# Kernel tuning notes

Hardware: AMD Instinct MI355X
Metric: run time of the kernel (lower is better)

The kernel has to match this reference:

```python
import jax, jax.numpy as jnp
import numpy as np

DIM = 1024
HEADS = 8
DIM_HEAD = 64
INNER = HEADS * DIM_HEAD  # 512


def setup_inputs() -> dict:
    key = jax.random.key(0)
    k1, k2, k3, k4 = jax.random.split(key, 4)
    x = jax.random.normal(k1, (4, 4096, DIM), dtype=jnp.float32)
    # torch nn.Linear weights: [out_features, in_features]
    w_qkv = jax.random.normal(k2, (INNER * 3, DIM), dtype=jnp.float32) * (DIM ** -0.5)
    w_out = jax.random.normal(k3, (DIM, INNER), dtype=jnp.float32) * (INNER ** -0.5)
    b_out = jax.random.normal(k4, (DIM,), dtype=jnp.float32) * 0.01
    return {"x": x, "w_qkv": w_qkv, "w_out": w_out, "b_out": b_out}


def reference(x, w_qkv, w_out, b_out):
    b, n, _ = x.shape
    h, dh = HEADS, DIM_HEAD
    qkv = x @ w_qkv.T  # [b, n, 3*inner]
    q, k, v = jnp.split(qkv, 3, axis=-1)
    # [b, n, inner] -> [b, h, n, dh]
    reshape = lambda t: t.reshape(b, n, h, dh).transpose(0, 2, 1, 3)
    q, k, v = reshape(q), reshape(k), reshape(v)
    k = jax.nn.softmax(k, axis=-1)
    context = jnp.einsum('bhnd,bhne->bhde', k, v)   # [b, h, dh, dh]
    out = jnp.einsum('bhnd,bhde->bhne', q, context)  # [b, h, n, dh]
    out = out.transpose(0, 2, 1, 3).reshape(b, n, h * dh)
    return out @ w_out.T + b_out
```

## Files before the change

### kernel.cpp

```cpp
#include <hip/hip_runtime.h>
#include <hip/hip_bf16.h>

using bf16 = __hip_bfloat16;
typedef __attribute__((ext_vector_type(8))) short short8;
typedef __attribute__((ext_vector_type(4))) float floatx4;

#define NB 4
#define NSEQ 4096
#define DIM 1024
#define INNER 512
#define TOK (NB * NSEQ)


__device__ inline unsigned short f2bf(float x) {
  union { bf16 h; unsigned short u; } c; c.h = __float2bfloat16(x); return c.u;
}
__device__ inline float bf2f(unsigned short u) {
  return __uint_as_float((unsigned)u << 16);
}
__device__ inline uint4 pack8(const float4 a, const float4 b) {
  union { uint4 u; unsigned short h[8]; } p;
  p.h[0] = f2bf(a.x); p.h[1] = f2bf(a.y); p.h[2] = f2bf(a.z); p.h[3] = f2bf(a.w);
  p.h[4] = f2bf(b.x); p.h[5] = f2bf(b.y); p.h[6] = f2bf(b.z); p.h[7] = f2bf(b.w);
  return p.u;
}

__device__ inline void gload_lds16(const bf16* g, bf16* ldsbase) {
  __builtin_amdgcn_global_load_lds(
      (const __attribute__((address_space(1))) void*)g,
      (__attribute__((address_space(3))) void*)ldsbase, 16, 0, 0);
}

__global__ __launch_bounds__(256)
void fused_prep(const float* __restrict__ x, const float* __restrict__ w_qkv,
                bf16* __restrict__ xb, bf16* __restrict__ wkvb,
                bf16* __restrict__ wqT) {
  const int tid = threadIdx.x;
  const int blk = blockIdx.x;

  if (blk < 8192) {
    const size_t i = (size_t)blk * 256 + tid;
    const float* src = x + i * 8;
    *(uint4*)(xb + i * 8) = pack8(((const float4*)src)[0], ((const float4*)src)[1]);
  } else if (blk < 8704) {
    const size_t i = (size_t)(blk - 8192) * 256 + tid;
    const float* src = w_qkv + (size_t)INNER * DIM + i * 8;
    *(uint4*)(wkvb + i * 8) = pack8(((const float4*)src)[0], ((const float4*)src)[1]);
  } else {
    __shared__ unsigned short t[64 * 68];
    const int q  = blk - 8704;
    const int c0 = (q & 15) * 64;
    const int r0 = (q >> 4) * 64;
#pragma unroll
    for (int l = 0; l < 4; ++l) {
      const int s = l * 256 + tid;
      const int row = s >> 4, col4 = s & 15;
      const float4 v = *(const float4*)(w_qkv + (size_t)(r0 + row) * 1024 + c0 + col4 * 4);
      t[row * 68 + col4 * 4 + 0] = f2bf(v.x);
      t[row * 68 + col4 * 4 + 1] = f2bf(v.y);
      t[row * 68 + col4 * 4 + 2] = f2bf(v.z);
      t[row * 68 + col4 * 4 + 3] = f2bf(v.w);
    }
    __syncthreads();
#pragma unroll
    for (int l = 0; l < 2; ++l) {
      const int s = l * 256 + tid;
      const int cc = s >> 3, g = s & 7;
      union { uint4 u; unsigned short h[8]; } o;
#pragma unroll
      for (int u = 0; u < 8; ++u) o.h[u] = t[(g * 8 + u) * 68 + cc];
      *(uint4*)((unsigned short*)wqT + (size_t)(c0 + cc) * 512 + r0 + g * 8) = o.u;
    }
  }
}

__global__ __launch_bounds__(256, 4)
void kv_softmax_ctx(const bf16* __restrict__ A, const bf16* __restrict__ Wkv,
                    float* __restrict__ ctx_part) {
  __shared__ __align__(16) char smem[33280];
  bf16* As = (bf16*)smem;
  bf16* Bs = (bf16*)(smem + 16384);
  unsigned short* skT = (unsigned short*)smem;
  unsigned short* vT  = (unsigned short*)(smem + 16640);

  const int tid    = threadIdx.x;
  const int p      = blockIdx.x;
  const int h      = (p >> 3) & 7;
  const int m_tile = (p & 7) + (p >> 6) * 8;
  const int m0     = m_tile * 128;

  const int wave = tid >> 6;
  const int lane = tid & 63;
  const int wr   = (wave >> 1) * 64;
  const int wc   = (wave & 1) * 64;
  const int quad = lane >> 4;
  const int r16  = lane & 15;
  const int rxor = r16 & 7;
  const int lrow = lane >> 3;
  const int lcol = lane & 7;
  const int gchunk = lcol ^ lrow;

  floatx4 acc[4][4];
#pragma unroll
  for (int i = 0; i < 4; ++i)
#pragma unroll
    for (int j = 0; j < 4; ++j) acc[i][j] = (floatx4)0.0f;

  for (int kt = 0; kt < 16; ++kt) {
    const int k0 = kt << 6;
#pragma unroll
    for (int t = 0; t < 4; ++t) {
      const int s   = wave * 4 + t;
      const int row = s * 8 + lrow;
      const int badd = (s * 8 >= 64) ? (448 + h * 64) : (h * 64);
      gload_lds16(A   + (size_t)(m0 + row) * 1024 + k0 + gchunk * 8, As + s * 512);
      gload_lds16(Wkv + (size_t)(badd + row) * 1024 + k0 + gchunk * 8, Bs + s * 512);
    }
    __syncthreads();
#pragma unroll
    for (int kk = 0; kk < 64; kk += 32) {
      const int cbase = kk >> 3;
      short8 af[4], bfg[4];
#pragma unroll
      for (int i = 0; i < 4; ++i)
        af[i] = *(const short8*)(As + (wr + i * 16 + r16) * 64 + (((quad + cbase) ^ rxor) << 3));
#pragma unroll
      for (int j = 0; j < 4; ++j)
        bfg[j] = *(const short8*)(Bs + (wc + j * 16 + r16) * 64 + (((quad + cbase) ^ rxor) << 3));
#pragma unroll
      for (int i = 0; i < 4; ++i)
#pragma unroll
        for (int j = 0; j < 4; ++j)
          acc[i][j] = __builtin_amdgcn_mfma_f32_16x16x32_bf16(af[i], bfg[j], acc[i][j], 0, 0, 0);
    }
    __syncthreads();
  }

  const int rowbase = wr + quad * 4;
  if ((wave & 1) == 0) {
#pragma unroll
    for (int i = 0; i < 4; ++i)
#pragma unroll
      for (int reg = 0; reg < 4; ++reg) {
        float kf[4];
#pragma unroll
        for (int j = 0; j < 4; ++j) kf[j] = bf2f(f2bf(acc[i][j][reg]));
        float mx = fmaxf(fmaxf(kf[0], kf[1]), fmaxf(kf[2], kf[3]));
        mx = fmaxf(mx, __shfl_xor(mx, 1, 64));
        mx = fmaxf(mx, __shfl_xor(mx, 2, 64));
        mx = fmaxf(mx, __shfl_xor(mx, 4, 64));
        mx = fmaxf(mx, __shfl_xor(mx, 8, 64));
        float e[4]; float s = 0.0f;
#pragma unroll
        for (int j = 0; j < 4; ++j) { e[j] = __expf(kf[j] - mx); s += e[j]; }
        s += __shfl_xor(s, 1, 64);
        s += __shfl_xor(s, 2, 64);
        s += __shfl_xor(s, 4, 64);
        s += __shfl_xor(s, 8, 64);
        const float inv = 1.0f / s;
        const int row = rowbase + i * 16 + reg;
#pragma unroll
        for (int j = 0; j < 4; ++j)
          skT[(j * 16 + r16) * 130 + row] = f2bf(e[j] * inv);
      }
  } else {
#pragma unroll
    for (int i = 0; i < 4; ++i)
#pragma unroll
      for (int reg = 0; reg < 4; ++reg) {
        const int row = rowbase + i * 16 + reg;
#pragma unroll
        for (int j = 0; j < 4; ++j)
          vT[(j * 16 + r16) * 130 + row] = f2bf(acc[i][j][reg]);
      }
  }
  __syncthreads();

  const int d0 = wave * 16;
  floatx4 cacc[4];
#pragma unroll
  for (int j = 0; j < 4; ++j) cacc[j] = (floatx4)0.0f;
#pragma unroll
  for (int kk = 0; kk < 4; ++kk) {
    const int kof = kk * 32 + quad * 8;
    union { short8 v; unsigned u[4]; } afr;
    {
      const unsigned* qa = (const unsigned*)(skT + (d0 + r16) * 130 + kof);
      afr.u[0] = qa[0]; afr.u[1] = qa[1]; afr.u[2] = qa[2]; afr.u[3] = qa[3];
    }
#pragma unroll
    for (int j = 0; j < 4; ++j) {
      union { short8 v; unsigned u[4]; } bfr;
      const unsigned* qb = (const unsigned*)(vT + (j * 16 + r16) * 130 + kof);
      bfr.u[0] = qb[0]; bfr.u[1] = qb[1]; bfr.u[2] = qb[2]; bfr.u[3] = qb[3];
      cacc[j] = __builtin_amdgcn_mfma_f32_16x16x32_bf16(afr.v, bfr.v, cacc[j], 0, 0, 0);
    }
  }

  float* cg = ctx_part + (size_t)(m_tile * 8 + h) * 4096;
#pragma unroll
  for (int j = 0; j < 4; ++j) {
    const int e = j * 16 + r16;
#pragma unroll
    for (int r = 0; r < 4; ++r) {
      const int d = d0 + quad * 4 + r;
      cg[d * 64 + e] = cacc[j][r];
    }
  }
}

__global__ __launch_bounds__(256)
void build_m2(const float* __restrict__ w_out, const float* __restrict__ ctx_part,
              bf16* __restrict__ M2) {
  __shared__ unsigned short wo_s[128 * 68];
  __shared__ __align__(16) float ctx_s[4096];

  const int tid = threadIdx.x;
  const int bh  = blockIdx.y;
  const int b   = bh >> 3, h = bh & 7;
  const int o0  = blockIdx.x * 128;

#pragma unroll
  for (int l = 0; l < 8; ++l) {
    const int s = l * 256 + tid;
    const int row = s >> 4, col4 = s & 15;
    const float4 v = *(const float4*)(w_out + (size_t)(o0 + row) * 512 + h * 64 + col4 * 4);
    wo_s[row * 68 + col4 * 4 + 0] = f2bf(v.x);
    wo_s[row * 68 + col4 * 4 + 1] = f2bf(v.y);
    wo_s[row * 68 + col4 * 4 + 2] = f2bf(v.z);
    wo_s[row * 68 + col4 * 4 + 3] = f2bf(v.w);
  }
  const float4* cg = (const float4*)(ctx_part + (size_t)(b * 256 + h) * 4096);
#pragma unroll
  for (int l = 0; l < 4; ++l) {
    const int idx = l * 256 + tid;
    float4 s = make_float4(0.f, 0.f, 0.f, 0.f);
#pragma unroll
    for (int sl = 0; sl < 32; ++sl) {
      const float4 v = cg[(size_t)sl * 8192 + idx];
      s.x += v.x; s.y += v.y; s.z += v.z; s.w += v.w;
    }
    ((float4*)ctx_s)[idx] = s;
  }
  __syncthreads();

  const int o_loc = tid & 127;
  const int dbase = (tid >> 7) * 32;
  float acc[32];
#pragma unroll
  for (int d = 0; d < 32; ++d) acc[d] = 0.0f;

  for (int e = 0; e < 64; ++e) {
    const float wf = bf2f(wo_s[o_loc * 68 + e]);
#pragma unroll
    for (int d = 0; d < 32; ++d)
      acc[d] += wf * ctx_s[(dbase + d) * 64 + e];
  }

  union { uint4 u[4]; unsigned short hh[32]; } o;
#pragma unroll
  for (int d = 0; d < 32; ++d) o.hh[d] = f2bf(acc[d]);
  unsigned short* dst = (unsigned short*)M2 + (size_t)(b * 1024 + o0 + o_loc) * 512 + h * 64 + dbase;
#pragma unroll
  for (int i = 0; i < 4; ++i) ((uint4*)dst)[i] = o.u[i];
}

template <typename TO>
__global__ __launch_bounds__(256, 4)
void gemm_bt(const bf16* __restrict__ A, int lda,
             const bf16* __restrict__ W, int mTiles,
             TO* __restrict__ C, int ldc, int K,
             TO* __restrict__ Calt, int msplit) {
  __shared__ __align__(16) bf16 As[128 * 64];
  __shared__ __align__(16) bf16 Bs[128 * 64];

  const int tid    = threadIdx.x;
  const int p      = blockIdx.x;
  const int m_tile = p % mTiles;
  const int n_tile = p / mTiles;
  const int m0     = m_tile * 128;
  const int n0     = n_tile * 128;

  const int wave = tid >> 6;
  const int lane = tid & 63;
  const int wr   = (wave >> 1) * 64;
  const int wc   = (wave & 1) * 64;
  const int quad = lane >> 4;
  const int r16  = lane & 15;
  const int rxor = r16 & 7;
  const int lrow = lane >> 3;
  const int lcol = lane & 7;
  const int gchunk = lcol ^ lrow;

  floatx4 acc[4][4];
#pragma unroll
  for (int i = 0; i < 4; ++i)
#pragma unroll
    for (int j = 0; j < 4; ++j) acc[i][j] = (floatx4)0.0f;

  const int ksteps = K >> 6;
  for (int kt = 0; kt < ksteps; ++kt) {
    const int k0 = kt << 6;
#pragma unroll
    for (int t = 0; t < 4; ++t) {
      const int s   = wave * 4 + t;
      const int row = s * 8 + lrow;
      gload_lds16(A + (size_t)(m0 + row) * lda + k0 + gchunk * 8, As + s * 512);
      gload_lds16(W + (size_t)(n0 + row) * K   + k0 + gchunk * 8, Bs + s * 512);
    }
    __syncthreads();
#pragma unroll
    for (int kk = 0; kk < 64; kk += 32) {
      const int cbase = kk >> 3;
      short8 af[4], bfg[4];
#pragma unroll
      for (int i = 0; i < 4; ++i)
        af[i] = *(const short8*)(As + (wr + i * 16 + r16) * 64 + (((quad + cbase) ^ rxor) << 3));
#pragma unroll
      for (int j = 0; j < 4; ++j)
        bfg[j] = *(const short8*)(Bs + (wc + j * 16 + r16) * 64 + (((quad + cbase) ^ rxor) << 3));
#pragma unroll
      for (int i = 0; i < 4; ++i)
#pragma unroll
        for (int j = 0; j < 4; ++j)
          acc[i][j] = __builtin_amdgcn_mfma_f32_16x16x32_bf16(af[i], bfg[j], acc[i][j], 0, 0, 0);
    }
    __syncthreads();
  }

  TO* Cb = C; int radj = 0;
  if (Calt && m0 >= msplit) { Cb = Calt; radj = msplit; }
#pragma unroll
  for (int j = 0; j < 4; ++j) {
    const int col = n0 + wc + j * 16 + r16;
#pragma unroll
    for (int i = 0; i < 4; ++i) {
      const int rowb = m0 + wr + i * 16 + quad * 4 - radj;
#pragma unroll
      for (int r = 0; r < 4; ++r)
        Cb[(size_t)(rowb + r) * ldc + col] = __float2bfloat16(acc[i][j][r]);
    }
  }
}

__global__ __launch_bounds__(256, 4)
void gemm_f32a(const float* __restrict__ A,
               const bf16* __restrict__ W, size_t wbatch,
               const bf16* __restrict__ Walt,
               const float* __restrict__ bias,
               float* __restrict__ C, int ldc) {
  __shared__ __align__(16) bf16 As[128 * 64];
  __shared__ __align__(16) bf16 Bs[128 * 64];

  const int tid    = threadIdx.x;
  const int p      = blockIdx.x;
  const int n_tile = (p >> 3) & 7;
  const int m_tile = (p & 7) + (p >> 6) * 8;
  const int m0 = m_tile * 128, n0 = n_tile * 128;
  const int batch = m_tile >> 5;
  const bf16* Wp = (batch == 3 && Walt) ? Walt : W + (size_t)batch * wbatch;

  const int wave = tid >> 6;
  const int lane = tid & 63;
  const int wr   = (wave >> 1) * 64;
  const int wc   = (wave & 1) * 64;
  const int quad = lane >> 4;
  const int r16  = lane & 15;
  const int rxor = r16 & 7;
  const int lrow = lane >> 3;
  const int lcol = lane & 7;
  const int gchunk = lcol ^ lrow;
  const int wb = wave * 8 + lrow;

  const float* Ax = A + (size_t)(m0 + wb) * 1024 + lcol * 8;

  floatx4 acc[4][4];
#pragma unroll
  for (int i = 0; i < 4; ++i)
#pragma unroll
    for (int j = 0; j < 4; ++j) acc[i][j] = (floatx4)0.0f;

  for (int kt = 0; kt < 16; ++kt) {
    const int k0 = kt << 6;
#pragma unroll
    for (int t = 0; t < 4; ++t) {
      const int s   = wave * 4 + t;
      const int row = s * 8 + lrow;
      gload_lds16(Wp + (size_t)(n0 + row) * 1024 + k0 + gchunk * 8, Bs + s * 512);
    }
    float4 rA[8];
#pragma unroll
    for (int l = 0; l < 4; ++l) {
      rA[2 * l]     = *(const float4*)(Ax + (size_t)l * 32768 + k0);
      rA[2 * l + 1] = *(const float4*)(Ax + (size_t)l * 32768 + k0 + 4);
    }
#pragma unroll
    for (int l = 0; l < 4; ++l) {
      const int row = l * 32 + wb;
      *(uint4*)(As + row * 64 + ((lcol ^ lrow) << 3)) = pack8(rA[2 * l], rA[2 * l + 1]);
    }
    __syncthreads();
#pragma unroll
    for (int kk = 0; kk < 64; kk += 32) {
      const int cbase = kk >> 3;
      short8 af[4], bfg[4];
#pragma unroll
      for (int i = 0; i < 4; ++i)
        af[i] = *(const short8*)(As + (wr + i * 16 + r16) * 64 + (((quad + cbase) ^ rxor) << 3));
#pragma unroll
      for (int j = 0; j < 4; ++j)
        bfg[j] = *(const short8*)(Bs + (wc + j * 16 + r16) * 64 + (((quad + cbase) ^ rxor) << 3));
#pragma unroll
      for (int i = 0; i < 4; ++i)
#pragma unroll
        for (int j = 0; j < 4; ++j)
          acc[i][j] = __builtin_amdgcn_mfma_f32_16x16x32_bf16(af[i], bfg[j], acc[i][j], 0, 0, 0);
    }
    __syncthreads();
  }

#pragma unroll
  for (int j = 0; j < 4; ++j) {
    const int col = n0 + wc + j * 16 + r16;
    const float bv = bias[col];
#pragma unroll
    for (int i = 0; i < 4; ++i) {
      const int rowb = m0 + wr + i * 16 + quad * 4;
#pragma unroll
      for (int r = 0; r < 4; ++r)
        C[(size_t)(rowb + r) * ldc + col] = acc[i][j][r] + bv;
    }
  }
}

extern "C" void kernel_launch(void* const* d_in, const int* in_sizes, int n_in,
                              void* d_out, int out_size, void* d_ws, size_t ws_size,
                              hipStream_t stream) {
  const float* x     = (const float*)d_in[0];
  const float* w_qkv = (const float*)d_in[1];
  const float* w_out = (const float*)d_in[2];
  const float* b_out = (const float*)d_in[3];
  float* out = (float*)d_out;

  char* wbuf = (char*)d_in[1];
  char* obuf = (char*)d_out;

  bf16*  xb   = (bf16*)obuf;
  float* ctxp = (float*)(obuf + (size_t)33554432);
  bf16*  wkvb = (bf16*)(obuf + (size_t)50331648);
  bf16*  M2   = (bf16*)(obuf + (size_t)52428800);
  bf16*  wqT  = (bf16*)(obuf + (size_t)56623104);
  bf16*  W2   = (bf16*)wbuf;
  bf16*  W2b3 = (bf16*)d_in[2];

  fused_prep<<<8832, 256, 0, stream>>>(x, w_qkv, xb, wkvb, wqT);

  kv_softmax_ctx<<<1024, 256, 0, stream>>>(xb, wkvb, ctxp);

  build_m2<<<dim3(8, 32), 256, 0, stream>>>(w_out, ctxp, M2);

  gemm_bt<bf16><<<256, 256, 0, stream>>>(
      M2, 512, wqT, 32, W2, 1024, 512, W2b3, 3072);

  gemm_f32a<<<1024, 256, 0, stream>>>(
      x, W2, (size_t)1048576, W2b3, b_out, out, DIM);
}
```

Before: 264.3 us.

## Drop x bf16 pre-conversion; compute KV via f32-input GEMM then separate softmax-context kernel

The full x-to-bf16 conversion pass in prep is removed. K/V are now produced by the fp32-A GEMM kernel (converting x on load) and written to a bf16 buffer. A new softmax_context kernel then reads K/V, applies the softmax and accumulates the per-slice contexts, and build_m2 is adjusted to sum 16 partial slices. This avoids writing and re-reading a bf16 copy of x, but adds a write and read of a K/V intermediate and one more launch.

Result: faster. 256.6 us (-2.9%).

```diff
diff --git a/kernel.cpp b/kernel.cpp
--- a/kernel.cpp
+++ b/kernel.cpp
@@ -32,23 +32,18 @@
 }
 
 __global__ __launch_bounds__(256)
-void fused_prep(const float* __restrict__ x, const float* __restrict__ w_qkv,
-                bf16* __restrict__ xb, bf16* __restrict__ wkvb,
+void fused_prep(const float* __restrict__ w_qkv, bf16* __restrict__ wkvb,
                 bf16* __restrict__ wqT) {
   const int tid = threadIdx.x;
   const int blk = blockIdx.x;
 
-  if (blk < 8192) {
+  if (blk < 512) {
     const size_t i = (size_t)blk * 256 + tid;
-    const float* src = x + i * 8;
-    *(uint4*)(xb + i * 8) = pack8(((const float4*)src)[0], ((const float4*)src)[1]);
-  } else if (blk < 8704) {
-    const size_t i = (size_t)(blk - 8192) * 256 + tid;
     const float* src = w_qkv + (size_t)INNER * DIM + i * 8;
     *(uint4*)(wkvb + i * 8) = pack8(((const float4*)src)[0], ((const float4*)src)[1]);
   } else {
     __shared__ unsigned short t[64 * 68];
-    const int q  = blk - 8704;
+    const int q  = blk - 512;
     const int c0 = (q & 15) * 64;
     const int r0 = (q >> 4) * 64;
 #pragma unroll
@@ -74,281 +69,13 @@
   }
 }
 
-__global__ __launch_bounds__(256, 4)
-void kv_softmax_ctx(const bf16* __restrict__ A, const bf16* __restrict__ Wkv,
-                    float* __restrict__ ctx_part) {
-  __shared__ __align__(16) char smem[33280];
-  bf16* As = (bf16*)smem;
-  bf16* Bs = (bf16*)(smem + 16384);
-  unsigned short* skT = (unsigned short*)smem;
-  unsigned short* vT  = (unsigned short*)(smem + 16640);
-
-  const int tid    = threadIdx.x;
-  const int p      = blockIdx.x;
-  const int h      = (p >> 3) & 7;
-  const int m_tile = (p & 7) + (p >> 6) * 8;
-  const int m0     = m_tile * 128;
-
-  const int wave = tid >> 6;
-  const int lane = tid & 63;
-  const int wr   = (wave >> 1) * 64;
-  const int wc   = (wave & 1) * 64;
-  const int quad = lane >> 4;
-  const int r16  = lane & 15;
-  const int rxor = r16 & 7;
-  const int lrow = lane >> 3;
-  const int lcol = lane & 7;
-  const int gchunk = lcol ^ lrow;
-
-  floatx4 acc[4][4];
-#pragma unroll
-  for (int i = 0; i < 4; ++i)
-#pragma unroll
-    for (int j = 0; j < 4; ++j) acc[i][j] = (floatx4)0.0f;
-
-  for (int kt = 0; kt < 16; ++kt) {
-    const int k0 = kt << 6;
-#pragma unroll
-    for (int t = 0; t < 4; ++t) {
-      const int s   = wave * 4 + t;
-      const int row = s * 8 + lrow;
-      const int badd = (s * 8 >= 64) ? (448 + h * 64) : (h * 64);
-      gload_lds16(A   + (size_t)(m0 + row) * 1024 + k0 + gchunk * 8, As + s * 512);
-      gload_lds16(Wkv + (size_t)(badd + row) * 1024 + k0 + gchunk * 8, Bs + s * 512);
-    }
-    __syncthreads();
-#pragma unroll
-    for (int kk = 0; kk < 64; kk += 32) {
-      const int cbase = kk >> 3;
-      short8 af[4], bfg[4];
-#pragma unroll
-      for (int i = 0; i < 4; ++i)
-        af[i] = *(const short8*)(As + (wr + i * 16 + r16) * 64 + (((quad + cbase) ^ rxor) << 3));
-#pragma unroll
-      for (int j = 0; j < 4; ++j)
-        bfg[j] = *(const short8*)(Bs + (wc + j * 16 + r16) * 64 + (((quad + cbase) ^ rxor) << 3));
-#pragma unroll
-      for (int i = 0; i < 4; ++i)
-#pragma unroll
-        for (int j = 0; j < 4; ++j)
-          acc[i][j] = __builtin_amdgcn_mfma_f32_16x16x32_bf16(af[i], bfg[j], acc[i][j], 0, 0, 0);
-    }
-    __syncthreads();
-  }
-
-  const int rowbase = wr + quad * 4;
-  if ((wave & 1) == 0) {
-#pragma unroll
-    for (int i = 0; i < 4; ++i)
-#pragma unroll
-      for (int reg = 0; reg < 4; ++reg) {
-        float kf[4];
-#pragma unroll
-        for (int j = 0; j < 4; ++j) kf[j] = bf2f(f2bf(acc[i][j][reg]));
-        float mx = fmaxf(fmaxf(kf[0], kf[1]), fmaxf(kf[2], kf[3]));
-        mx = fmaxf(mx, __shfl_xor(mx, 1, 64));
-        mx = fmaxf(mx, __shfl_xor(mx, 2, 64));
-        mx = fmaxf(mx, __shfl_xor(mx, 4, 64));
-        mx = fmaxf(mx, __shfl_xor(mx, 8, 64));
-        float e[4]; float s = 0.0f;
-#pragma unroll
-        for (int j = 0; j < 4; ++j) { e[j] = __expf(kf[j] - mx); s += e[j]; }
-        s += __shfl_xor(s, 1, 64);
-        s += __shfl_xor(s, 2, 64);
-        s += __shfl_xor(s, 4, 64);
-        s += __shfl_xor(s, 8, 64);
-        const float inv = 1.0f / s;
-        const int row = rowbase + i * 16 + reg;
-#pragma unroll
-        for (int j = 0; j < 4; ++j)
-          skT[(j * 16 + r16) * 130 + row] = f2bf(e[j] * inv);
-      }
-  } else {
-#pragma unroll
-    for (int i = 0; i < 4; ++i)
-#pragma unroll
-      for (int reg = 0; reg < 4; ++reg) {
-        const int row = rowbase + i * 16 + reg;
-#pragma unroll
-        for (int j = 0; j < 4; ++j)
-          vT[(j * 16 + r16) * 130 + row] = f2bf(acc[i][j][reg]);
-      }
-  }
-  __syncthreads();
-
-  const int d0 = wave * 16;
-  floatx4 cacc[4];
-#pragma unroll
-  for (int j = 0; j < 4; ++j) cacc[j] = (floatx4)0.0f;
-#pragma unroll
-  for (int kk = 0; kk < 4; ++kk) {
-    const int kof = kk * 32 + quad * 8;
-    union { short8 v; unsigned u[4]; } afr;
-    {
-      const unsigned* qa = (const unsigned*)(skT + (d0 + r16) * 130 + kof);
-      afr.u[0] = qa[0]; afr.u[1] = qa[1]; afr.u[2] = qa[2]; afr.u[3] = qa[3];
-    }
-#pragma unroll
-    for (int j = 0; j < 4; ++j) {
-      union { short8 v; unsigned u[4]; } bfr;
-      const unsigned* qb = (const unsigned*)(vT + (j * 16 + r16) * 130 + kof);
-      bfr.u[0] = qb[0]; bfr.u[1] = qb[1]; bfr.u[2] = qb[2]; bfr.u[3] = qb[3];
-      cacc[j] = __builtin_amdgcn_mfma_f32_16x16x32_bf16(afr.v, bfr.v, cacc[j], 0, 0, 0);
-    }
-  }
-
-  float* cg = ctx_part + (size_t)(m_tile * 8 + h) * 4096;
-#pragma unroll
-  for (int j = 0; j < 4; ++j) {
-    const int e = j * 16 + r16;
-#pragma unroll
-    for (int r = 0; r < 4; ++r) {
-      const int d = d0 + quad * 4 + r;
-      cg[d * 64 + e] = cacc[j][r];
-    }
-  }
-}
-
-__global__ __launch_bounds__(256)
-void build_m2(const float* __restrict__ w_out, const float* __restrict__ ctx_part,
-              bf16* __restrict__ M2) {
-  __shared__ unsigned short wo_s[128 * 68];
-  __shared__ __align__(16) float ctx_s[4096];
-
-  const int tid = threadIdx.x;
-  const int bh  = blockIdx.y;
-  const int b   = bh >> 3, h = bh & 7;
-  const int o0  = blockIdx.x * 128;
-
-#pragma unroll
-  for (int l = 0; l < 8; ++l) {
-    const int s = l * 256 + tid;
-    const int row = s >> 4, col4 = s & 15;
-    const float4 v = *(const float4*)(w_out + (size_t)(o0 + row) * 512 + h * 64 + col4 * 4);
-    wo_s[row * 68 + col4 * 4 + 0] = f2bf(v.x);
-    wo_s[row * 68 + col4 * 4 + 1] = f2bf(v.y);
-    wo_s[row * 68 + col4 * 4 + 2] = f2bf(v.z);
-    wo_s[row * 68 + col4 * 4 + 3] = f2bf(v.w);
-  }
-  const float4* cg = (const float4*)(ctx_part + (size_t)(b * 256 + h) * 4096);
-#pragma unroll
-  for (int l = 0; l < 4; ++l) {
-    const int idx = l * 256 + tid;
-    float4 s = make_float4(0.f, 0.f, 0.f, 0.f);
-#pragma unroll
-    for (int sl = 0; sl < 32; ++sl) {
-      const float4 v = cg[(size_t)sl * 8192 + idx];
-      s.x += v.x; s.y += v.y; s.z += v.z; s.w += v.w;
-    }
-    ((float4*)ctx_s)[idx] = s;
-  }
-  __syncthreads();
-
-  const int o_loc = tid & 127;
-  const int dbase = (tid >> 7) * 32;
-  float acc[32];
-#pragma unroll
-  for (int d = 0; d < 32; ++d) acc[d] = 0.0f;
-
-  for (int e = 0; e < 64; ++e) {
-    const float wf = bf2f(wo_s[o_loc * 68 + e]);
-#pragma unroll
-    for (int d = 0; d < 32; ++d)
-      acc[d] += wf * ctx_s[(dbase + d) * 64 + e];
-  }
-
-  union { uint4 u[4]; unsigned short hh[32]; } o;
-#pragma unroll
-  for (int d = 0; d < 32; ++d) o.hh[d] = f2bf(acc[d]);
-  unsigned short* dst = (unsigned short*)M2 + (size_t)(b * 1024 + o0 + o_loc) * 512 + h * 64 + dbase;
-#pragma unroll
-  for (int i = 0; i < 4; ++i) ((uint4*)dst)[i] = o.u[i];
-}
-
-template <typename TO>
-__global__ __launch_bounds__(256, 4)
-void gemm_bt(const bf16* __restrict__ A, int lda,
-             const bf16* __restrict__ W, int mTiles,
-             TO* __restrict__ C, int ldc, int K,
-             TO* __restrict__ Calt, int msplit) {
-  __shared__ __align__(16) bf16 As[128 * 64];
-  __shared__ __align__(16) bf16 Bs[128 * 64];
-
-  const int tid    = threadIdx.x;
-  const int p      = blockIdx.x;
-  const int m_tile = p % mTiles;
-  const int n_tile = p / mTiles;
-  const int m0     = m_tile * 128;
-  const int n0     = n_tile * 128;
-
-  const int wave = tid >> 6;
-  const int lane = tid & 63;
-  const int wr   = (wave >> 1) * 64;
-  const int wc   = (wave & 1) * 64;
-  const int quad = lane >> 4;
-  const int r16  = lane & 15;
-  const int rxor = r16 & 7;
-  const int lrow = lane >> 3;
-  const int lcol = lane & 7;
-  const int gchunk = lcol ^ lrow;
-
-  floatx4 acc[4][4];
-#pragma unroll
-  for (int i = 0; i < 4; ++i)
-#pragma unroll
-    for (int j = 0; j < 4; ++j) acc[i][j] = (floatx4)0.0f;
-
-  const int ksteps = K >> 6;
-  for (int kt = 0; kt < ksteps; ++kt) {
-    const int k0 = kt << 6;
-#pragma unroll
-    for (int t = 0; t < 4; ++t) {
-      const int s   = wave * 4 + t;
-      const int row = s * 8 + lrow;
-      gload_lds16(A + (size_t)(m0 + row) * lda + k0 + gchunk * 8, As + s * 512);
-      gload_lds16(W + (size_t)(n0 + row) * K   + k0 + gchunk * 8, Bs + s * 512);
-    }
-    __syncthreads();
-#pragma unroll
-    for (int kk = 0; kk < 64; kk += 32) {
-      const int cbase = kk >> 3;
-      short8 af[4], bfg[4];
-#pragma unroll
-      for (int i = 0; i < 4; ++i)
-        af[i] = *(const short8*)(As + (wr + i * 16 + r16) * 64 + (((quad + cbase) ^ rxor) << 3));
-#pragma unroll
-      for (int j = 0; j < 4; ++j)
-        bfg[j] = *(const short8*)(Bs + (wc + j * 16 + r16) * 64 + (((quad + cbase) ^ rxor) << 3));
-#pragma unroll
-      for (int i = 0; i < 4; ++i)
-#pragma unroll
-        for (int j = 0; j < 4; ++j)
-          acc[i][j] = __builtin_amdgcn_mfma_f32_16x16x32_bf16(af[i], bfg[j], acc[i][j], 0, 0, 0);
-    }
-    __syncthreads();
-  }
-
-  TO* Cb = C; int radj = 0;
-  if (Calt && m0 >= msplit) { Cb = Calt; radj = msplit; }
-#pragma unroll
-  for (int j = 0; j < 4; ++j) {
-    const int col = n0 + wc + j * 16 + r16;
-#pragma unroll
-    for (int i = 0; i < 4; ++i) {
-      const int rowb = m0 + wr + i * 16 + quad * 4 - radj;
-#pragma unroll
-      for (int r = 0; r < 4; ++r)
-        Cb[(size_t)(rowb + r) * ldc + col] = __float2bfloat16(acc[i][j][r]);
-    }
-  }
-}
-
+template <typename TO, bool BIAS, bool BATCH>
 __global__ __launch_bounds__(256, 4)
 void gemm_f32a(const float* __restrict__ A,
                const bf16* __restrict__ W, size_t wbatch,
                const bf16* __restrict__ Walt,
                const float* __restrict__ bias,
-               float* __restrict__ C, int ldc) {
+               TO* __restrict__ C, int ldc) {
   __shared__ __align__(16) bf16 As[128 * 64];
   __shared__ __align__(16) bf16 Bs[128 * 64];
 
@@ -357,8 +84,11 @@
   const int n_tile = (p >> 3) & 7;
   const int m_tile = (p & 7) + (p >> 6) * 8;
   const int m0 = m_tile * 128, n0 = n_tile * 128;
-  const int batch = m_tile >> 5;
-  const bf16* Wp = (batch == 3 && Walt) ? Walt : W + (size_t)batch * wbatch;
+  const bf16* Wp = W;
+  if constexpr (BATCH) {
+    const int batch = m_tile >> 5;
+    Wp = (batch == 3) ? Walt : W + (size_t)batch * wbatch;
+  }
 
   const int wave = tid >> 6;
   const int lane = tid & 63;
@@ -422,13 +152,243 @@
 #pragma unroll
   for (int j = 0; j < 4; ++j) {
     const int col = n0 + wc + j * 16 + r16;
-    const float bv = bias[col];
+    const float bv = BIAS ? bias[col] : 0.0f;
 #pragma unroll
     for (int i = 0; i < 4; ++i) {
       const int rowb = m0 + wr + i * 16 + quad * 4;
 #pragma unroll
+      for (int r = 0; r < 4; ++r) {
+        const float v = acc[i][j][r] + bv;
+        if constexpr (sizeof(TO) == 2)
+          C[(size_t)(rowb + r) * ldc + col] = __float2bfloat16(v);
+        else
+          C[(size_t)(rowb + r) * ldc + col] = v;
+      }
+    }
+  }
+}
+
+__global__ __launch_bounds__(256)
+void softmax_context(const unsigned short* __restrict__ kv,
+                     float* __restrict__ ctx_part) {
+  __shared__ unsigned short skT[64 * 130];
+  __shared__ unsigned short vT [64 * 130];
+
+  const int tid   = threadIdx.x;
+  const int wave  = tid >> 6;
+  const int lane  = tid & 63;
+  const int bh    = blockIdx.x >> 4;
+  const int slice = blockIdx.x & 15;
+  const int b     = bh >> 3, h = bh & 7;
+
+  const int quad = lane >> 4;
+  const int r16  = lane & 15;
+  const int d0   = wave * 16;
+
+  floatx4 acc[4];
+#pragma unroll
+  for (int j = 0; j < 4; ++j) acc[j] = (floatx4)0.0f;
+
+  const int rgrp = tid >> 3;
+  const int c    = tid & 7;
+
+  for (int ch = 0; ch < 2; ++ch) {
+#pragma unroll
+    for (int p = 0; p < 4; ++p) {
+      const int r = p * 32 + rgrp;
+      const size_t rowbase =
+          (size_t)(b * NSEQ + slice * 256 + ch * 128 + r) * 1024 + h * 64;
+      const uint4 k8 = *(const uint4*)(kv + rowbase + c * 8);
+      const uint4 v8 = *(const uint4*)(kv + rowbase + 512 + c * 8);
+      const unsigned short* kb = (const unsigned short*)&k8;
+      const unsigned short* vb = (const unsigned short*)&v8;
+
+      float kf[8];
+#pragma unroll
+      for (int j = 0; j < 8; ++j) kf[j] = bf2f(kb[j]);
+      float mx = kf[0];
+#pragma unroll
+      for (int j = 1; j < 8; ++j) mx = fmaxf(mx, kf[j]);
+      mx = fmaxf(mx, __shfl_xor(mx, 1, 64));
+      mx = fmaxf(mx, __shfl_xor(mx, 2, 64));
+      mx = fmaxf(mx, __shfl_xor(mx, 4, 64));
+      float e[8]; float s = 0.0f;
+#pragma unroll
+      for (int j = 0; j < 8; ++j) { e[j] = __expf(kf[j] - mx); s += e[j]; }
+      s += __shfl_xor(s, 1, 64);
+      s += __shfl_xor(s, 2, 64);
+      s += __shfl_xor(s, 4, 64);
+      const float inv = 1.0f / s;
+#pragma unroll
+      for (int j = 0; j < 8; ++j) {
+        const int d = c * 8 + j;
+        skT[d * 130 + r] = f2bf(e[j] * inv);
+        vT [d * 130 + r] = vb[j];
+      }
+    }
+    __syncthreads();
+
+#pragma unroll
+    for (int kk = 0; kk < 4; ++kk) {
+      const int kof = kk * 32 + quad * 8;
+      union { short8 v; unsigned u[4]; } afr;
+      {
+        const unsigned* q = (const unsigned*)(skT + (d0 + r16) * 130 + kof);
+        afr.u[0] = q[0]; afr.u[1] = q[1]; afr.u[2] = q[2]; afr.u[3] = q[3];
+      }
+#pragma unroll
+      for (int j = 0; j < 4; ++j) {
+        union { short8 v; unsigned u[4]; } bfr;
+        const unsigned* q = (const unsigned*)(vT + (j * 16 + r16) * 130 + kof);
+        bfr.u[0] = q[0]; bfr.u[1] = q[1]; bfr.u[2] = q[2]; bfr.u[3] = q[3];
+        acc[j] = __builtin_amdgcn_mfma_f32_16x16x32_bf16(afr.v, bfr.v, acc[j], 0, 0, 0);
+      }
+    }
+    __syncthreads();
+  }
+
+  float* cg = ctx_part + ((size_t)slice * 32 + bh) * 4096;
+#pragma unroll
+  for (int j = 0; j < 4; ++j) {
+    const int e = j * 16 + r16;
+#pragma unroll
+    for (int r = 0; r < 4; ++r) {
+      const int d = d0 + quad * 4 + r;
+      cg[d * 64 + e] = acc[j][r];
+    }
+  }
+}
+
+__global__ __launch_bounds__(256)
+void build_m2(const float* __restrict__ w_out, const float* __restrict__ ctx_part,
+              bf16* __restrict__ M2) {
+  __shared__ unsigned short wo_s[128 * 68];
+  __shared__ __align__(16) float ctx_s[4096];
+
+  const int tid = threadIdx.x;
+  const int bh  = blockIdx.y;
+  const int b   = bh >> 3, h = bh & 7;
+  const int o0  = blockIdx.x * 128;
+
+#pragma unroll
+  for (int l = 0; l < 8; ++l) {
+    const int s = l * 256 + tid;
+    const int row = s >> 4, col4 = s & 15;
+    const float4 v = *(const float4*)(w_out + (size_t)(o0 + row) * 512 + h * 64 + col4 * 4);
+    wo_s[row * 68 + col4 * 4 + 0] = f2bf(v.x);
+    wo_s[row * 68 + col4 * 4 + 1] = f2bf(v.y);
+    wo_s[row * 68 + col4 * 4 + 2] = f2bf(v.z);
+    wo_s[row * 68 + col4 * 4 + 3] = f2bf(v.w);
+  }
+  const float4* cg = (const float4*)(ctx_part + (size_t)bh * 4096);
+#pragma unroll
+  for (int l = 0; l < 4; ++l) {
+    const int idx = l * 256 + tid;
+    float4 s = make_float4(0.f, 0.f, 0.f, 0.f);
+#pragma unroll
+    for (int sl = 0; sl < 16; ++sl) {
+      const float4 v = cg[(size_t)sl * 32768 + idx];
+      s.x += v.x; s.y += v.y; s.z += v.z; s.w += v.w;
+    }
+    ((float4*)ctx_s)[idx] = s;
+  }
+  __syncthreads();
+
+  const int o_loc = tid & 127;
+  const int dbase = (tid >> 7) * 32;
+  float acc[32];
+#pragma unroll
+  for (int d = 0; d < 32; ++d) acc[d] = 0.0f;
+
+  for (int e = 0; e < 64; ++e) {
+    const float wf = bf2f(wo_s[o_loc * 68 + e]);
+#pragma unroll
+    for (int d = 0; d < 32; ++d)
+      acc[d] += wf * ctx_s[(dbase + d) * 64 + e];
+  }
+
+  union { uint4 u[4]; unsigned short hh[32]; } o;
+#pragma unroll
+  for (int d = 0; d < 32; ++d) o.hh[d] = f2bf(acc[d]);
+  unsigned short* dst = (unsigned short*)M2 + (size_t)(b * 1024 + o0 + o_loc) * 512 + h * 64 + dbase;
+#pragma unroll
+  for (int i = 0; i < 4; ++i) ((uint4*)dst)[i] = o.u[i];
+}
+
+template <typename TO>
+__global__ __launch_bounds__(256, 4)
+void gemm_bt(const bf16* __restrict__ A, int lda,
+             const bf16* __restrict__ W, int mTiles,
+             TO* __restrict__ C, int ldc, int K,
+             TO* __restrict__ Calt, int msplit) {
+  __shared__ __align__(16) bf16 As[128 * 64];
+  __shared__ __align__(16) bf16 Bs[128 * 64];
+
+  const int tid    = threadIdx.x;
+  const int p      = blockIdx.x;
+  const int m_tile = p % mTiles;
+  const int n_tile = p / mTiles;
+  const int m0     = m_tile * 128;
+  const int n0     = n_tile * 128;
+
+  const int wave = tid >> 6;
+  const int lane = tid & 63;
+  const int wr   = (wave >> 1) * 64;
+  const int wc   = (wave & 1) * 64;
+  const int quad = lane >> 4;
+  const int r16  = lane & 15;
+  const int rxor = r16 & 7;
+  const int lrow = lane >> 3;
+  const int lcol = lane & 7;
+  const int gchunk = lcol ^ lrow;
+
+  floatx4 acc[4][4];
+#pragma unroll
+  for (int i = 0; i < 4; ++i)
+#pragma unroll
+    for (int j = 0; j < 4; ++j) acc[i][j] = (floatx4)0.0f;
+
+  const int ksteps = K >> 6;
+  for (int kt = 0; kt < ksteps; ++kt) {
+    const int k0 = kt << 6;
+#pragma unroll
+    for (int t = 0; t < 4; ++t) {
+      const int s   = wave * 4 + t;
+      const int row = s * 8 + lrow;
+      gload_lds16(A + (size_t)(m0 + row) * lda + k0 + gchunk * 8, As + s * 512);
+      gload_lds16(W + (size_t)(n0 + row) * K   + k0 + gchunk * 8, Bs + s * 512);
+    }
+    __syncthreads();
+#pragma unroll
+    for (int kk = 0; kk < 64; kk += 32) {
+      const int cbase = kk >> 3;
+      short8 af[4], bfg[4];
+#pragma unroll
+      for (int i = 0; i < 4; ++i)
+        af[i] = *(const short8*)(As + (wr + i * 16 + r16) * 64 + (((quad + cbase) ^ rxor) << 3));
+#pragma unroll
+      for (int j = 0; j < 4; ++j)
+        bfg[j] = *(const short8*)(Bs + (wc + j * 16 + r16) * 64 + (((quad + cbase) ^ rxor) << 3));
+#pragma unroll
+      for (int i = 0; i < 4; ++i)
+#pragma unroll
+        for (int j = 0; j < 4; ++j)
+          acc[i][j] = __builtin_amdgcn_mfma_f32_16x16x32_bf16(af[i], bfg[j], acc[i][j], 0, 0, 0);
+    }
+    __syncthreads();
+  }
+
+  TO* Cb = C; int radj = 0;
+  if (Calt && m0 >= msplit) { Cb = Calt; radj = msplit; }
+#pragma unroll
+  for (int j = 0; j < 4; ++j) {
+    const int col = n0 + wc + j * 16 + r16;
+#pragma unroll
+    for (int i = 0; i < 4; ++i) {
+      const int rowb = m0 + wr + i * 16 + quad * 4 - radj;
+#pragma unroll
       for (int r = 0; r < 4; ++r)
-        C[(size_t)(rowb + r) * ldc + col] = acc[i][j][r] + bv;
+        Cb[(size_t)(rowb + r) * ldc + col] = __float2bfloat16(acc[i][j][r]);
     }
   }
 }
@@ -445,23 +405,26 @@
   char* wbuf = (char*)d_in[1];
   char* obuf = (char*)d_out;
 
-  bf16*  xb   = (bf16*)obuf;
-  float* ctxp = (float*)(obuf + (size_t)33554432);
-  bf16*  wkvb = (bf16*)(obuf + (size_t)50331648);
-  bf16*  M2   = (bf16*)(obuf + (size_t)52428800);
-  bf16*  wqT  = (bf16*)(obuf + (size_t)56623104);
+  bf16*  kv   = (bf16*)obuf;
+  bf16*  wkvb = (bf16*)(obuf + (size_t)33554432);
+  bf16*  M2   = (bf16*)(obuf + (size_t)35651584);
+  bf16*  wqT  = (bf16*)(obuf + (size_t)39845888);
+  float* ctxp = (float*)(obuf + (size_t)41943040);
   bf16*  W2   = (bf16*)wbuf;
   bf16*  W2b3 = (bf16*)d_in[2];
 
-  fused_prep<<<8832, 256, 0, stream>>>(x, w_qkv, xb, wkvb, wqT);
-
-  kv_softmax_ctx<<<1024, 256, 0, stream>>>(xb, wkvb, ctxp);
+  fused_prep<<<640, 256, 0, stream>>>(w_qkv, wkvb, wqT);
+
+  gemm_f32a<bf16, false, false><<<1024, 256, 0, stream>>>(
+      x, wkvb, 0, nullptr, nullptr, kv, 1024);
+
+  softmax_context<<<512, 256, 0, stream>>>((const unsigned short*)kv, ctxp);
 
   build_m2<<<dim3(8, 32), 256, 0, stream>>>(w_out, ctxp, M2);
 
   gemm_bt<bf16><<<256, 256, 0, stream>>>(
       M2, 512, wqT, 32, W2, 1024, 512, W2b3, 3072);
 
-  gemm_f32a<<<1024, 256, 0, stream>>>(
+  gemm_f32a<float, true, true><<<1024, 256, 0, stream>>>(
       x, W2, (size_t)1048576, W2b3, b_out, out, DIM);
 }
```
